# Kernel optimization log

Measured on AMD Instinct MI355X. Metric: run time of the kernel, lower is better.

## Reference

```python
import jax, jax.numpy as jnp
import numpy as np


def setup_inputs() -> dict:
    key = jax.random.key(0)
    ks = jax.random.split(key, 5)
    B, H, W, C = 4, 64, 64, 256
    Ck = C // 8  # key/query channels = 32
    x = jax.random.normal(ks[0], (B, H, W, C), dtype=jnp.float32)
    # 1x1 conv kernels (spec_norm=False -> plain conv), Glorot-ish scaling
    Wf = jax.random.normal(ks[1], (C, Ck), dtype=jnp.float32) * (1.0 / np.sqrt(C))
    Wg = jax.random.normal(ks[2], (C, Ck), dtype=jnp.float32) * (1.0 / np.sqrt(C))
    Wh = jax.random.normal(ks[3], (C, C), dtype=jnp.float32) * (1.0 / np.sqrt(C))
    bf = jnp.zeros((Ck,), dtype=jnp.float32)
    bg = jnp.zeros((Ck,), dtype=jnp.float32)
    bh = jnp.zeros((C,), dtype=jnp.float32)
    # gamma is zero-init in the module; use a nonzero value so the attention
    # branch actually contributes to the output (as after some training).
    gamma = jnp.float32(0.5)
    return {"x": x, "Wf": Wf, "bf": bf, "Wg": Wg, "bg": bg,
            "Wh": Wh, "bh": bh, "gamma": gamma}


def reference(x, Wf, bf, Wg, bg, Wh, bh, gamma):
    B, H, W, C = x.shape
    N = H * W
    xf = x.reshape(B, N, C)  # hw_flatten of input (1x1 conv == per-pixel matmul)
    f = xf @ Wf + bf         # [B, N, Ck] keys
    g = xf @ Wg + bg         # [B, N, Ck] queries
    h = xf @ Wh + bh         # [B, N, C]  values
    s = jnp.einsum('bqk,bnk->bqn', g, f)  # [B, N, N] scores (g @ f^T)
    b = jax.nn.softmax(s, axis=-1)
    o = jnp.einsum('bqn,bnc->bqc', b, h)  # [B, N, C]
    # in-channels == nfilters, so scale(x) = x (identity)
    y = gamma * o.reshape(B, H, W, C) + x
    return y
```

## Files before the change

### kernel.cpp

```cpp
#include <hip/hip_runtime.h>
#include <stdint.h>

#define B_ 4
#define N_ 4096
#define C_ 256
#define LOG2E 1.44269504088896340736f
#define SOFT_OFF 88.0f

typedef float f32x4 __attribute__((ext_vector_type(4)));
typedef float f32x16 __attribute__((ext_vector_type(16)));
typedef short s16x8 __attribute__((ext_vector_type(8)));
typedef __bf16 bf16x8 __attribute__((ext_vector_type(8)));
typedef _Float16 f16x8 __attribute__((ext_vector_type(8)));

static __device__ __forceinline__ unsigned short f2bf(float f) {
    union { float f; uint32_t u; } v; v.f = f;
    return (unsigned short)((v.u + 0x7FFFu + ((v.u >> 16) & 1u)) >> 16);
}
static __device__ __forceinline__ unsigned short f2bf_rh(float f) {
    union { float f; uint32_t u; } v; v.f = f;
    return (unsigned short)((v.u + 0x8000u) >> 16);
}

__global__ __launch_bounds__(256) void wprep(
    const float* __restrict__ Wf, const float* __restrict__ Wg,
    const float* __restrict__ Wh, _Float16* __restrict__ WT)
{
    __shared__ float tile[64][33];
    const int t = blockIdx.x, kc = blockIdx.y, tid = threadIdx.x;
    const float* src; int stride;
    if (t == 0)      { src = Wf;                stride = 32;  }
    else if (t == 1) { src = Wg;                stride = 32;  }
    else             { src = Wh + (t - 2) * 32; stride = 256; }

    const int c = tid & 31, a = tid >> 5;
    #pragma unroll
    for (int p = 0; p < 8; p++) {
        int kk = p * 8 + a;
        tile[kk][c] = src[(size_t)(kc * 64 + kk) * stride + c];
    }
    __syncthreads();
    const int kk = tid & 63, aa = tid >> 6;
    #pragma unroll
    for (int p = 0; p < 8; p++) {
        int cc = p * 4 + aa;
        WT[(size_t)(t * 32 + cc) * 256 + kc * 64 + kk] = (_Float16)tile[kk][cc];
    }
}

__global__ __launch_bounds__(512, 2) void proj_kernel(
    const float* __restrict__ x,
    const float* __restrict__ bfp, const float* __restrict__ bgp,
    const float* __restrict__ bhp,
    const _Float16* __restrict__ WT,
    _Float16* __restrict__ qf16, _Float16* __restrict__ kf16,
    unsigned short* __restrict__ v_frag)
{
    __shared__ __align__(16) _Float16 xs[64 * 256];
    __shared__ __align__(16) unsigned short tbuf[8][32 * 40];

    const int tid  = threadIdx.x;
    const int lane = tid & 63;
    const int wave = tid >> 6;
    const int m_   = lane & 31;
    const int k8   = lane >> 5;
    const int row0 = blockIdx.x * 64;
    const int b    = row0 >> 12;
    const int n0   = row0 & 4095;
    const int kt   = n0 >> 6;

    #pragma unroll
    for (int i = 0; i < 4; i++) {
        int r  = 16 * i + (tid >> 5);
        int c5 = tid & 31;
        const f32x4* src = (const f32x4*)(x + (size_t)(row0 + r) * 256 + c5 * 8);
        f32x4 a = src[0], c4 = src[1];
        f16x8 h = { (_Float16)a.x, (_Float16)a.y, (_Float16)a.z, (_Float16)a.w,
                    (_Float16)c4.x, (_Float16)c4.y, (_Float16)c4.z, (_Float16)c4.w };
        int chunk = (((r >> 5) * 32 + c5)) * 32 + ((r & 31) ^ (c5 & 7));
        *(f16x8*)(xs + chunk * 8) = h;
    }
    __syncthreads();

    const int rowsub = wave & 1;
    const int grp    = wave >> 1;
    const int ntile  = (grp < 2) ? 3 : 2;
    const int t_base = (grp < 2) ? grp * 3 : 6 + (grp - 2) * 2;
    const _Float16* wb[3];
    #pragma unroll
    for (int t = 0; t < 3; t++)
        wb[t] = WT + (size_t)((t_base + (t < ntile ? t : 0)) * 32 + m_) * 256 + k8 * 8;

    f32x16 acc[3];
    #pragma unroll
    for (int t = 0; t < 3; t++)
        #pragma unroll
        for (int i = 0; i < 16; i++) acc[t][i] = 0.f;

    f16x8 Bb[2][4][3];
    #pragma unroll
    for (int j = 0; j < 4; j++)
        #pragma unroll
        for (int t = 0; t < 3; t++) {
            if (t >= ntile) break;
            Bb[0][j][t] = *(const f16x8*)(wb[t] + j * 16);
        }
    #pragma unroll
    for (int g4 = 0; g4 < 4; g4++) {
        const int cur = g4 & 1, nxt = cur ^ 1;
        if (g4 < 3)
            #pragma unroll
            for (int j = 0; j < 4; j++)
                #pragma unroll
                for (int t = 0; t < 3; t++) {
                    if (t >= ntile) break;
                    Bb[nxt][j][t] = *(const f16x8*)(wb[t] + (g4 * 4 + 4 + j) * 16);
                }
        #pragma unroll
        for (int j = 0; j < 4; j++) {
            int ks = g4 * 4 + j;
            f16x8 A = *(const f16x8*)(xs + ((rowsub * 32 + ks * 2 + k8) * 32
                                            + (m_ ^ ((ks * 2 + k8) & 7))) * 8);
            #pragma unroll
            for (int t = 0; t < 3; t++) {
                if (t >= ntile) break;
                acc[t] = __builtin_amdgcn_mfma_f32_32x32x16_f16(A, Bb[cur][j][t],
                                                                acc[t], 0, 0, 0);
            }
        }
    }

    #pragma unroll
    for (int t = 0; t < 3; t++) {
        if (t >= ntile) break;
        const int tile = t_base + t;
        if (tile < 2) {
            float bias = (tile == 0) ? bfp[m_] : bgp[m_];
            _Float16* dst = (tile == 0) ? kf16 : qf16;
            #pragma unroll
            for (int r = 0; r < 16; r++) {
                int m = (r & 3) + 8 * (r >> 2) + 4 * k8;
                int row = row0 + rowsub * 32 + m;
                dst[(size_t)row * 32 + m_] = (_Float16)(acc[t][r] + bias);
            }
        } else {
            const int ht   = tile - 2;
            const int chgv = ht >> 2, chslv = ht & 3;
            float bias = bhp[ht * 32 + m_];
            unsigned short* buf = tbuf[wave];
            #pragma unroll
            for (int u = 0; u < 8; u++) {
                int r = 2 * u;
                int m = (r & 3) + 8 * (r >> 2) + 4 * k8;
                uint32_t v = (uint32_t)f2bf(acc[t][r] + bias)
                           | ((uint32_t)f2bf(acc[t][r + 1] + bias) << 16);
                *(uint32_t*)(buf + m_ * 40 + m) = v;
            }
            #pragma unroll
            for (int u = 0; u < 2; u++) {
                int idx2 = u * 64 + lane;
                int chr = idx2 >> 2, q8 = idx2 & 3;
                s16x8 vv = *(const s16x8*)(buf + chr * 40 + q8 * 8);
                int oct = rowsub * 4 + q8;
                size_t e = (((((size_t)(b * 2 + chgv) * 64 + kt) * 8 + oct) * 4
                              + chslv) * 32 + chr) * 8;
                *(s16x8*)(v_frag + e) = vv;
            }
        }
    }
}

__global__ __launch_bounds__(1024, 4) void attn_kernel(
    const _Float16* __restrict__ qf16, const _Float16* __restrict__ kf16,
    const unsigned short* __restrict__ v_frag,
    const float* __restrict__ x, const float* __restrict__ gamma_p,
    float* __restrict__ out)
{
    __shared__ __align__(16) unsigned short P_s[2][2][4096];
    __shared__ float l_s[2][4][32];

    const int tid  = threadIdx.x;
    const int lane = tid & 63;
    const int wave = tid >> 6;
    const int qsub = wave & 1;
    const int j    = wave >> 1;
    const int m_   = lane & 31;
    const int k8   = lane >> 5;
    const int qt   = blockIdx.x;
    const int b    = blockIdx.y;
    const size_t bn = (size_t)b * N_;
    const bool is_s = (wave < 8);
    const int ksl  = j;
    const int octw = ksl * 4 + (m_ >> 3);
    const int osw  = octw & 3;
    const int kofs = m_ & 7;

    const unsigned short* vb = v_frag + (size_t)(b * 2 + (j >> 2)) * 524288
                             + (j & 3) * 256 + m_ * 8;

    const int qrow = qt * 64 + qsub * 32 + m_;
    const f16x8 Aq0 = *(const f16x8*)(qf16 + (bn + qrow) * 32 + k8 * 8);
    const f16x8 Aq1 = *(const f16x8*)(qf16 + (bn + qrow) * 32 + 16 + k8 * 8);

    f16x8 Kc0 = {}, Kc1 = {};
    if (is_s) {
        const _Float16* kp = kf16 + (bn + ksl * 32 + m_) * 32;
        Kc0 = *(const f16x8*)(kp + k8 * 8);
        Kc1 = *(const f16x8*)(kp + 16 + k8 * 8);
    }
    bf16x8 Bv0[4], Bv1[4];
    #pragma unroll
    for (int ks = 0; ks < 4; ks++)
        Bv0[ks] = *(const bf16x8*)(vb + (ks * 2 + k8) * 1024);

    f32x16 acc;
    float l_acc[16];
    #pragma unroll
    for (int i = 0; i < 16; i++) { acc[i] = 0.f; l_acc[i] = 0.f; }

    for (int it = 0; it < 32; it++) {
        const int par = it & 1;
        const int itn = (it < 31) ? it + 1 : 31;
        f16x8 Kn0 = {}, Kn1 = {};
        if (is_s) {
            const _Float16* kp = kf16 + (bn + itn * 128 + ksl * 32 + m_) * 32;
            Kn0 = *(const f16x8*)(kp + k8 * 8);
            Kn1 = *(const f16x8*)(kp + 16 + k8 * 8);
            f32x16 s;
            #pragma unroll
            for (int i = 0; i < 16; i++) s[i] = 0.f;
            s = __builtin_amdgcn_mfma_f32_32x32x16_f16(Aq0, Kc0, s, 0, 0, 0);
            s = __builtin_amdgcn_mfma_f32_32x32x16_f16(Aq1, Kc1, s, 0, 0, 0);
            unsigned short* Pb = P_s[par][qsub];
            #pragma unroll
            for (int r = 0; r < 16; r++) {
                float p = __builtin_amdgcn_exp2f(fmaf(s[r], LOG2E, -SOFT_OFF));
                l_acc[r] += p;
                int q = (r & 3) + 8 * (r >> 2) + 4 * k8;
                Pb[(octw * 32 + (q ^ osw)) * 8 + kofs] = f2bf_rh(p);
            }
        }
        __syncthreads();

        const unsigned short* Pr = P_s[par][qsub];
        #pragma unroll
        for (int ks = 0; ks < 4; ks++)
            Bv1[ks] = *(const bf16x8*)(vb + (size_t)it * 16384 + 8192
                                       + (ks * 2 + k8) * 1024);
        #pragma unroll
        for (int ks = 0; ks < 4; ks++) {
            int oct = ks * 2 + k8;
            bf16x8 Ap = *(const bf16x8*)(Pr + (oct * 32 + (m_ ^ (oct & 3))) * 8);
            acc = __builtin_amdgcn_mfma_f32_32x32x16_bf16(Ap, Bv0[ks], acc, 0, 0, 0);
        }
        #pragma unroll
        for (int ks = 0; ks < 4; ks++) {
            int oct = 8 + ks * 2 + k8;
            bf16x8 Ap = *(const bf16x8*)(Pr + (oct * 32 + (m_ ^ (oct & 3))) * 8);
            acc = __builtin_amdgcn_mfma_f32_32x32x16_bf16(Ap, Bv1[ks], acc, 0, 0, 0);
        }
        #pragma unroll
        for (int ks = 0; ks < 4; ks++)
            Bv0[ks] = *(const bf16x8*)(vb + (size_t)itn * 16384
                                       + (ks * 2 + k8) * 1024);
        if (is_s) { Kc0 = Kn0; Kc1 = Kn1; }
    }

    if (is_s) {
        #pragma unroll
        for (int off = 1; off < 32; off <<= 1)
            #pragma unroll
            for (int r = 0; r < 16; r++)
                l_acc[r] += __shfl_xor(l_acc[r], off, 64);
        if (m_ == 0) {
            #pragma unroll
            for (int r = 0; r < 16; r++) {
                int q = (r & 3) + 8 * (r >> 2) + 4 * k8;
                l_s[qsub][ksl][q] = l_acc[r];
            }
        }
    }
    __syncthreads();

    const float gamma = *gamma_p;
    #pragma unroll
    for (int r = 0; r < 16; r++) {
        int q = (r & 3) + 8 * (r >> 2) + 4 * k8;
        float l = l_s[qsub][0][q] + l_s[qsub][1][q]
                + l_s[qsub][2][q] + l_s[qsub][3][q];
        size_t idx = (bn + qt * 64 + qsub * 32 + q) * 256 + j * 32 + m_;
        out[idx] = gamma * (acc[r] / l) + x[idx];
    }
}

extern "C" void kernel_launch(void* const* d_in, const int* in_sizes, int n_in,
                              void* d_out, int out_size, void* d_ws, size_t ws_size,
                              hipStream_t stream) {
    const float* x   = (const float*)d_in[0];
    const float* Wf  = (const float*)d_in[1];
    const float* bfp = (const float*)d_in[2];
    const float* Wg  = (const float*)d_in[3];
    const float* bgp = (const float*)d_in[4];
    const float* Wh  = (const float*)d_in[5];
    const float* bhp = (const float*)d_in[6];
    const float* gam = (const float*)d_in[7];
    float* out = (float*)d_out;

    unsigned char* ws = (unsigned char*)d_ws;
    const size_t MB = 1 << 20;
    _Float16* WT    = (_Float16*)(ws);
    _Float16* qf16  = (_Float16*)(ws + 1 * MB);
    _Float16* kf16  = (_Float16*)(ws + 2 * MB);
    unsigned short* v_frag = (unsigned short*)(ws + 3 * MB);

    wprep<<<dim3(10, 4), dim3(256), 0, stream>>>(Wf, Wg, Wh, WT);
    proj_kernel<<<dim3(256), dim3(512), 0, stream>>>(
        x, bfp, bgp, bhp, WT, qf16, kf16, v_frag);
    attn_kernel<<<dim3(64, 4), dim3(1024), 0, stream>>>(
        qf16, kf16, v_frag, x, gam, out);
}
```

Baseline: 151.4 us.

## Spread score computation across all waves and process two key tiles per barrier

Before, only 8 of the 16 waves computed QK scores and softmax numerators while the others sat idle at the barrier. Now every wave computes a 32-key score slice, so each iteration covers 256 keys and the loop runs 16 times instead of 32, halving the number of block-wide barriers. The shared P buffer doubles in size, the row-sum partials are reduced over 8 slices, and value fragment loads are re-staged across the two half-tiles. The cost is more LDS per block and more register pressure from the extra prefetches, which could reduce occupancy.

```diff
diff --git a/kernel.cpp b/kernel.cpp
--- a/kernel.cpp
+++ b/kernel.cpp
@@ -176,8 +176,8 @@
     const float* __restrict__ x, const float* __restrict__ gamma_p,
     float* __restrict__ out)
 {
-    __shared__ __align__(16) unsigned short P_s[2][2][4096];
-    __shared__ float l_s[2][4][32];
+    __shared__ __align__(16) unsigned short P_s[2][2][8192];
+    __shared__ float l_s[2][8][32];
 
     const int tid  = threadIdx.x;
     const int lane = tid & 63;
@@ -189,8 +189,8 @@
     const int qt   = blockIdx.x;
     const int b    = blockIdx.y;
     const size_t bn = (size_t)b * N_;
-    const bool is_s = (wave < 8);
-    const int ksl  = j;
+    const int h_   = j >> 2;
+    const int ksl  = j & 3;
     const int octw = ksl * 4 + (m_ >> 3);
     const int osw  = octw & 3;
     const int kofs = m_ & 7;
@@ -202,82 +202,98 @@
     const f16x8 Aq0 = *(const f16x8*)(qf16 + (bn + qrow) * 32 + k8 * 8);
     const f16x8 Aq1 = *(const f16x8*)(qf16 + (bn + qrow) * 32 + 16 + k8 * 8);
 
-    f16x8 Kc0 = {}, Kc1 = {};
-    if (is_s) {
-        const _Float16* kp = kf16 + (bn + ksl * 32 + m_) * 32;
-        Kc0 = *(const f16x8*)(kp + k8 * 8);
-        Kc1 = *(const f16x8*)(kp + 16 + k8 * 8);
-    }
-    bf16x8 Bv0[4], Bv1[4];
+    const _Float16* kjb = kf16 + (bn + j * 32 + m_) * 32;
+    f16x8 Kc0 = *(const f16x8*)(kjb + k8 * 8);
+    f16x8 Kc1 = *(const f16x8*)(kjb + 16 + k8 * 8);
+
+    bf16x8 BvA[4], BvB[4];
     #pragma unroll
     for (int ks = 0; ks < 4; ks++)
-        Bv0[ks] = *(const bf16x8*)(vb + (ks * 2 + k8) * 1024);
+        BvA[ks] = *(const bf16x8*)(vb + (ks * 2 + k8) * 1024);
 
     f32x16 acc;
     float l_acc[16];
     #pragma unroll
     for (int i = 0; i < 16; i++) { acc[i] = 0.f; l_acc[i] = 0.f; }
 
-    for (int it = 0; it < 32; it++) {
+    for (int it = 0; it < 16; it++) {
         const int par = it & 1;
-        const int itn = (it < 31) ? it + 1 : 31;
-        f16x8 Kn0 = {}, Kn1 = {};
-        if (is_s) {
-            const _Float16* kp = kf16 + (bn + itn * 128 + ksl * 32 + m_) * 32;
-            Kn0 = *(const f16x8*)(kp + k8 * 8);
-            Kn1 = *(const f16x8*)(kp + 16 + k8 * 8);
-            f32x16 s;
-            #pragma unroll
-            for (int i = 0; i < 16; i++) s[i] = 0.f;
-            s = __builtin_amdgcn_mfma_f32_32x32x16_f16(Aq0, Kc0, s, 0, 0, 0);
-            s = __builtin_amdgcn_mfma_f32_32x32x16_f16(Aq1, Kc1, s, 0, 0, 0);
-            unsigned short* Pb = P_s[par][qsub];
-            #pragma unroll
-            for (int r = 0; r < 16; r++) {
-                float p = __builtin_amdgcn_exp2f(fmaf(s[r], LOG2E, -SOFT_OFF));
-                l_acc[r] += p;
-                int q = (r & 3) + 8 * (r >> 2) + 4 * k8;
-                Pb[(octw * 32 + (q ^ osw)) * 8 + kofs] = f2bf_rh(p);
-            }
+        const int itn = (it < 15) ? it + 1 : 15;
+        f16x8 Kn0 = *(const f16x8*)(kjb + itn * 8192 + k8 * 8);
+        f16x8 Kn1 = *(const f16x8*)(kjb + itn * 8192 + 16 + k8 * 8);
+
+        f32x16 s;
+        #pragma unroll
+        for (int i = 0; i < 16; i++) s[i] = 0.f;
+        s = __builtin_amdgcn_mfma_f32_32x32x16_f16(Aq0, Kc0, s, 0, 0, 0);
+        s = __builtin_amdgcn_mfma_f32_32x32x16_f16(Aq1, Kc1, s, 0, 0, 0);
+        unsigned short* Pb = P_s[par][qsub] + h_ * 4096;
+        #pragma unroll
+        for (int r = 0; r < 16; r++) {
+            float p = __builtin_amdgcn_exp2f(fmaf(s[r], LOG2E, -SOFT_OFF));
+            l_acc[r] += p;
+            int q = (r & 3) + 8 * (r >> 2) + 4 * k8;
+            Pb[(octw * 32 + (q ^ osw)) * 8 + kofs] = f2bf_rh(p);
         }
         __syncthreads();
 
         const unsigned short* Pr = P_s[par][qsub];
+        const size_t kvt = (size_t)it * 2;
         #pragma unroll
         for (int ks = 0; ks < 4; ks++)
-            Bv1[ks] = *(const bf16x8*)(vb + (size_t)it * 16384 + 8192
+            BvB[ks] = *(const bf16x8*)(vb + kvt * 16384 + 8192
                                        + (ks * 2 + k8) * 1024);
         #pragma unroll
         for (int ks = 0; ks < 4; ks++) {
             int oct = ks * 2 + k8;
             bf16x8 Ap = *(const bf16x8*)(Pr + (oct * 32 + (m_ ^ (oct & 3))) * 8);
-            acc = __builtin_amdgcn_mfma_f32_32x32x16_bf16(Ap, Bv0[ks], acc, 0, 0, 0);
-        }
+            acc = __builtin_amdgcn_mfma_f32_32x32x16_bf16(Ap, BvA[ks], acc, 0, 0, 0);
+        }
+        #pragma unroll
+        for (int ks = 0; ks < 4; ks++)
+            BvA[ks] = *(const bf16x8*)(vb + (kvt + 1) * 16384
+                                       + (ks * 2 + k8) * 1024);
         #pragma unroll
         for (int ks = 0; ks < 4; ks++) {
             int oct = 8 + ks * 2 + k8;
             bf16x8 Ap = *(const bf16x8*)(Pr + (oct * 32 + (m_ ^ (oct & 3))) * 8);
-            acc = __builtin_amdgcn_mfma_f32_32x32x16_bf16(Ap, Bv1[ks], acc, 0, 0, 0);
+            acc = __builtin_amdgcn_mfma_f32_32x32x16_bf16(Ap, BvB[ks], acc, 0, 0, 0);
         }
         #pragma unroll
         for (int ks = 0; ks < 4; ks++)
-            Bv0[ks] = *(const bf16x8*)(vb + (size_t)itn * 16384
+            BvB[ks] = *(const bf16x8*)(vb + (kvt + 1) * 16384 + 8192
                                        + (ks * 2 + k8) * 1024);
-        if (is_s) { Kc0 = Kn0; Kc1 = Kn1; }
-    }
-
-    if (is_s) {
-        #pragma unroll
-        for (int off = 1; off < 32; off <<= 1)
-            #pragma unroll
-            for (int r = 0; r < 16; r++)
-                l_acc[r] += __shfl_xor(l_acc[r], off, 64);
-        if (m_ == 0) {
-            #pragma unroll
-            for (int r = 0; r < 16; r++) {
-                int q = (r & 3) + 8 * (r >> 2) + 4 * k8;
-                l_s[qsub][ksl][q] = l_acc[r];
-            }
+        #pragma unroll
+        for (int ks = 0; ks < 4; ks++) {
+            int oct = ks * 2 + k8;
+            bf16x8 Ap = *(const bf16x8*)(Pr + 4096
+                                         + (oct * 32 + (m_ ^ (oct & 3))) * 8);
+            acc = __builtin_amdgcn_mfma_f32_32x32x16_bf16(Ap, BvA[ks], acc, 0, 0, 0);
+        }
+        #pragma unroll
+        for (int ks = 0; ks < 4; ks++) {
+            int oct = 8 + ks * 2 + k8;
+            bf16x8 Ap = *(const bf16x8*)(Pr + 4096
+                                         + (oct * 32 + (m_ ^ (oct & 3))) * 8);
+            acc = __builtin_amdgcn_mfma_f32_32x32x16_bf16(Ap, BvB[ks], acc, 0, 0, 0);
+        }
+        #pragma unroll
+        for (int ks = 0; ks < 4; ks++)
+            BvA[ks] = *(const bf16x8*)(vb + (size_t)itn * 2 * 16384
+                                       + (ks * 2 + k8) * 1024);
+        Kc0 = Kn0; Kc1 = Kn1;
+    }
+
+    #pragma unroll
+    for (int off = 1; off < 32; off <<= 1)
+        #pragma unroll
+        for (int r = 0; r < 16; r++)
+            l_acc[r] += __shfl_xor(l_acc[r], off, 64);
+    if (m_ == 0) {
+        #pragma unroll
+        for (int r = 0; r < 16; r++) {
+            int q = (r & 3) + 8 * (r >> 2) + 4 * k8;
+            l_s[qsub][j][q] = l_acc[r];
         }
     }
     __syncthreads();
@@ -286,8 +302,10 @@
     #pragma unroll
     for (int r = 0; r < 16; r++) {
         int q = (r & 3) + 8 * (r >> 2) + 4 * k8;
-        float l = l_s[qsub][0][q] + l_s[qsub][1][q]
-                + l_s[qsub][2][q] + l_s[qsub][3][q];
+        float l = ((l_s[qsub][0][q] + l_s[qsub][1][q])
+                 + (l_s[qsub][2][q] + l_s[qsub][3][q]))
+                + ((l_s[qsub][4][q] + l_s[qsub][5][q])
+                 + (l_s[qsub][6][q] + l_s[qsub][7][q]));
         size_t idx = (bn + qt * 64 + qsub * 32 + q) * 256 + j * 32 + m_;
         out[idx] = gamma * (acc[r] / l) + x[idx];
     }
```

Result: slower. 157.3 us (+3.9%).

## Split key dimension across wave pairs so each P fragment feeds two channel tiles

Applied to the files above, without the earlier changes.

Waves now each own half of the 128-key step and two 32-channel output tiles, instead of the full key step for a single channel tile. Each P fragment read from LDS is reused for two MFMAs, halving LDS reads of P per MFMA. The two key-halves' partial accumulators are combined through a new shared-memory buffer at the end. This adds 64KB of shared memory, which may reduce occupancy, and adds a cross-wave reduction step.

```diff
diff --git a/kernel.cpp b/kernel.cpp
--- a/kernel.cpp
+++ b/kernel.cpp
@@ -178,25 +178,27 @@
 {
     __shared__ __align__(16) unsigned short P_s[2][2][4096];
     __shared__ float l_s[2][4][32];
+    __shared__ __align__(16) float accs[2][4][2][32][32];
 
     const int tid  = threadIdx.x;
     const int lane = tid & 63;
     const int wave = tid >> 6;
     const int qsub = wave & 1;
-    const int j    = wave >> 1;
+    const int h_   = (wave >> 1) & 1;
+    const int cp   = wave >> 2;
     const int m_   = lane & 31;
     const int k8   = lane >> 5;
     const int qt   = blockIdx.x;
     const int b    = blockIdx.y;
     const size_t bn = (size_t)b * N_;
-    const bool is_s = (wave < 8);
-    const int ksl  = j;
+    const bool is_s = (cp < 2);
+    const int ksl  = h_ * 2 + cp;
     const int octw = ksl * 4 + (m_ >> 3);
     const int osw  = octw & 3;
     const int kofs = m_ & 7;
 
-    const unsigned short* vb = v_frag + (size_t)(b * 2 + (j >> 2)) * 524288
-                             + (j & 3) * 256 + m_ * 8;
+    const unsigned short* vbh = v_frag + (size_t)(b * 2 + (cp >> 1)) * 524288
+                              + ((cp & 1) * 2) * 256 + m_ * 8 + h_ * 8192;
 
     const int qrow = qt * 64 + qsub * 32 + m_;
     const f16x8 Aq0 = *(const f16x8*)(qf16 + (bn + qrow) * 32 + k8 * 8);
@@ -208,15 +210,17 @@
         Kc0 = *(const f16x8*)(kp + k8 * 8);
         Kc1 = *(const f16x8*)(kp + 16 + k8 * 8);
     }
-    bf16x8 Bv0[4], Bv1[4];
-    #pragma unroll
-    for (int ks = 0; ks < 4; ks++)
-        Bv0[ks] = *(const bf16x8*)(vb + (ks * 2 + k8) * 1024);
-
-    f32x16 acc;
+    bf16x8 BvA[2][2], BvB[2][2];
+    #pragma unroll
+    for (int ks = 0; ks < 2; ks++)
+        #pragma unroll
+        for (int c = 0; c < 2; c++)
+            BvA[ks][c] = *(const bf16x8*)(vbh + (ks * 2 + k8) * 1024 + c * 256);
+
+    f32x16 acc[2];
     float l_acc[16];
     #pragma unroll
-    for (int i = 0; i < 16; i++) { acc[i] = 0.f; l_acc[i] = 0.f; }
+    for (int i = 0; i < 16; i++) { acc[0][i] = 0.f; acc[1][i] = 0.f; l_acc[i] = 0.f; }
 
     for (int it = 0; it < 32; it++) {
         const int par = it & 1;
@@ -243,26 +247,37 @@
         __syncthreads();
 
         const unsigned short* Pr = P_s[par][qsub];
-        #pragma unroll
-        for (int ks = 0; ks < 4; ks++)
-            Bv1[ks] = *(const bf16x8*)(vb + (size_t)it * 16384 + 8192
-                                       + (ks * 2 + k8) * 1024);
-        #pragma unroll
-        for (int ks = 0; ks < 4; ks++) {
-            int oct = ks * 2 + k8;
-            bf16x8 Ap = *(const bf16x8*)(Pr + (oct * 32 + (m_ ^ (oct & 3))) * 8);
-            acc = __builtin_amdgcn_mfma_f32_32x32x16_bf16(Ap, Bv0[ks], acc, 0, 0, 0);
-        }
-        #pragma unroll
-        for (int ks = 0; ks < 4; ks++) {
-            int oct = 8 + ks * 2 + k8;
-            bf16x8 Ap = *(const bf16x8*)(Pr + (oct * 32 + (m_ ^ (oct & 3))) * 8);
-            acc = __builtin_amdgcn_mfma_f32_32x32x16_bf16(Ap, Bv1[ks], acc, 0, 0, 0);
-        }
-        #pragma unroll
-        for (int ks = 0; ks < 4; ks++)
-            Bv0[ks] = *(const bf16x8*)(vb + (size_t)itn * 16384
-                                       + (ks * 2 + k8) * 1024);
+        const unsigned short* vit = vbh + (size_t)it * 16384;
+        #pragma unroll
+        for (int ks = 0; ks < 2; ks++)
+            #pragma unroll
+            for (int c = 0; c < 2; c++)
+                BvB[ks][c] = *(const bf16x8*)(vit + ((ks + 2) * 2 + k8) * 1024
+                                              + c * 256);
+        #pragma unroll
+        for (int ks = 0; ks < 2; ks++) {
+            int o = h_ * 8 + ks * 2 + k8;
+            bf16x8 Ap = *(const bf16x8*)(Pr + (o * 32 + (m_ ^ (o & 3))) * 8);
+            acc[0] = __builtin_amdgcn_mfma_f32_32x32x16_bf16(Ap, BvA[ks][0],
+                                                             acc[0], 0, 0, 0);
+            acc[1] = __builtin_amdgcn_mfma_f32_32x32x16_bf16(Ap, BvA[ks][1],
+                                                             acc[1], 0, 0, 0);
+        }
+        #pragma unroll
+        for (int ks = 0; ks < 2; ks++) {
+            int o = h_ * 8 + (ks + 2) * 2 + k8;
+            bf16x8 Ap = *(const bf16x8*)(Pr + (o * 32 + (m_ ^ (o & 3))) * 8);
+            acc[0] = __builtin_amdgcn_mfma_f32_32x32x16_bf16(Ap, BvB[ks][0],
+                                                             acc[0], 0, 0, 0);
+            acc[1] = __builtin_amdgcn_mfma_f32_32x32x16_bf16(Ap, BvB[ks][1],
+                                                             acc[1], 0, 0, 0);
+        }
+        #pragma unroll
+        for (int ks = 0; ks < 2; ks++)
+            #pragma unroll
+            for (int c = 0; c < 2; c++)
+                BvA[ks][c] = *(const bf16x8*)(vbh + (size_t)itn * 16384
+                                              + (ks * 2 + k8) * 1024 + c * 256);
         if (is_s) { Kc0 = Kn0; Kc1 = Kn1; }
     }
 
@@ -280,16 +295,24 @@
             }
         }
     }
+    #pragma unroll
+    for (int r = 0; r < 16; r++) {
+        int q = (r & 3) + 8 * (r >> 2) + 4 * k8;
+        accs[qsub][cp][h_][q][m_] = acc[h_][r];
+    }
     __syncthreads();
 
     const float gamma = *gamma_p;
+    const int sl = 1 - h_;
     #pragma unroll
     for (int r = 0; r < 16; r++) {
         int q = (r & 3) + 8 * (r >> 2) + 4 * k8;
         float l = l_s[qsub][0][q] + l_s[qsub][1][q]
                 + l_s[qsub][2][q] + l_s[qsub][3][q];
-        size_t idx = (bn + qt * 64 + qsub * 32 + q) * 256 + j * 32 + m_;
-        out[idx] = gamma * (acc[r] / l) + x[idx];
+        float v = acc[sl][r] + accs[qsub][cp][sl][q][m_];
+        size_t idx = (bn + qt * 64 + qsub * 32 + q) * 256
+                   + cp * 64 + sl * 32 + m_;
+        out[idx] = gamma * (v / l) + x[idx];
     }
 }
 
```

Measured after the change: 168.5 us. 11.3% more time.
